# Performance work log

Hardware: AMD Instinct MI355X
Metric: run time of the kernel (lower is better)

## Reference

```python
import jax, jax.numpy as jnp
import numpy as np

BN_EPS = 1e-5


def _bn(x, g, b, m, v):
    # inference-mode BatchNorm1d over channel dim of [B, C, N]
    return g[:, None] * (x - m[:, None]) * jax.lax.rsqrt(v[:, None] + BN_EPS) + b[:, None]


def _conv1x1(w, x):
    # Conv1d kernel_size=1, no bias: [O, C] x [B, C, N] -> [B, O, N]
    return jnp.einsum('oc,bcn->bon', w, x)


def setup_inputs() -> dict:
    key = jax.random.key(0)
    ks = jax.random.split(key, 32)
    B, N = 8, 4096

    def w(k, sh):
        return jax.random.normal(k, sh, jnp.float32) * 0.05

    def bn_params(k, c):
        k0, k1, k2, k3 = jax.random.split(k, 4)
        g = 1.0 + 0.1 * jax.random.normal(k0, (c,), jnp.float32)
        b = 0.1 * jax.random.normal(k1, (c,), jnp.float32)
        m = 0.1 * jax.random.normal(k2, (c,), jnp.float32)
        v = jax.random.uniform(k3, (c,), jnp.float32, 0.5, 1.5)
        return g, b, m, v

    g1, b1, m1, v1 = bn_params(ks[2], 64)
    gq, bq, mq, vq = bn_params(ks[3], 16)
    gk, bk, mk, vk = bn_params(ks[4], 16)
    gv, bv, mv, vv = bn_params(ks[5], 3)

    return {
        'x': jax.random.normal(ks[0], (B, 3, N), jnp.float32),
        'w1': w(ks[6], (64, 3)),
        'g1': g1, 'b1': b1, 'm1': m1, 'v1': v1,
        'w2': w(ks[7], (128, 64)),
        'wq': w(ks[8], (16, 128)),
        'gq': gq, 'bq': bq, 'mq': mq, 'vq': vq,
        'wk': w(ks[9], (16, 128)),
        'gk': gk, 'bk': bk, 'mk': mk, 'vk': vk,
        'wv': w(ks[10], (3, 128)),
        'gv': gv, 'bv': bv, 'mv': mv, 'vv': vv,
        'alpha': 0.1 * jax.random.normal(ks[11], (1,), jnp.float32),
        'offset': 0.1 * jax.random.normal(ks[12], (1,), jnp.float32),
    }


def reference(x, w1, g1, b1, m1, v1, w2,
              wq, gq, bq, mq, vq,
              wk, gk, bk, mk, vk,
              wv, gv, bv, mv, vv,
              alpha, offset):
    # mlp: conv(3->64) -> BN -> ReLU -> conv(64->128)
    feat = _conv1x1(w2, jax.nn.relu(_bn(_conv1x1(w1, x + offset), g1, b1, m1, v1)))  # [B,128,N]
    q = jax.nn.relu(_bn(_conv1x1(wq, feat), gq, bq, mq, vq))  # [B,16,N]
    k = jax.nn.relu(_bn(_conv1x1(wk, feat), gk, bk, mk, vk))  # [B,16,N]
    energy = jnp.einsum('bcn,bcm->bnm', q, k)                 # [B,N,N] (Q^T K)
    sim = jax.nn.softmax(energy, axis=-1)
    # offset-attention: column-wise L1 renormalization
    sim = sim / (1e-9 + sim.sum(axis=1, keepdims=True))
    v_ = jax.nn.relu(_bn(_conv1x1(wv, feat), gv, bv, mv, vv))  # [B,3,N]
    out = jnp.einsum('bcn,bnm->bcm', v_, sim)                  # [B,3,N]
    return alpha * out + x
```

## Files before the change

### kernel.cpp

```cpp
#include <hip/hip_runtime.h>

#define NPTS 4096
#define NB   8
#define BN_EPS 1e-5f
#define LOG2E 1.4426950408889634f
#define RS_SLICES 8
#define CS_SLICES 4

typedef float f32x16 __attribute__((ext_vector_type(16)));
typedef short bf16x8 __attribute__((ext_vector_type(8)));
typedef unsigned short ushort_t;

#if __has_builtin(__builtin_amdgcn_exp2f)
#define EXP2(x) __builtin_amdgcn_exp2f(x)
#else
#define EXP2(x) exp2f(x)
#endif

__device__ __forceinline__ ushort_t f2bf(float f) {
    unsigned u = __builtin_bit_cast(unsigned, f);
    unsigned r = (u + 0x7FFFu + ((u >> 16) & 1u)) >> 16;
    return (ushort_t)r;
}

__global__ __launch_bounds__(256) void k0_prep(
    const float* __restrict__ w1, const float* __restrict__ g1, const float* __restrict__ b1,
    const float* __restrict__ m1, const float* __restrict__ v1,
    const float* __restrict__ w2,
    const float* __restrict__ wq, const float* __restrict__ gq, const float* __restrict__ bq,
    const float* __restrict__ mq, const float* __restrict__ vq,
    const float* __restrict__ wk, const float* __restrict__ gk, const float* __restrict__ bk,
    const float* __restrict__ mk, const float* __restrict__ vk,
    const float* __restrict__ wv, const float* __restrict__ gv, const float* __restrict__ bv,
    const float* __restrict__ mv, const float* __restrict__ vv,
    float* __restrict__ Wc, float* __restrict__ tb,
    float* __restrict__ w1s, float* __restrict__ t1)
{
    const int j = blockIdx.x;
    const int t = threadIdx.x;
    if (j == 35) {
        if (t < 64) {
            float s = g1[t] * rsqrtf(v1[t] + BN_EPS);
            w1s[t*3+0] = s * w1[t*3+0];
            w1s[t*3+1] = s * w1[t*3+1];
            w1s[t*3+2] = s * w1[t*3+2];
            t1[t] = b1[t] - s * m1[t];
        }
        return;
    }
    __shared__ float red[256];
    const int c = t & 63;
    const int chunk = t >> 6;
    const float* wrow;
    float g, bb, mm, vr, post = 1.f;
    if (j < 16)      { wrow = wq + j*128;      g = gq[j];    bb = bq[j];    mm = mq[j];    vr = vq[j];    post = LOG2E; }
    else if (j < 32) { int u = j-16; wrow = wk + u*128; g = gk[u]; bb = bk[u]; mm = mk[u]; vr = vk[u]; }
    else             { int u = j-32; wrow = wv + u*128; g = gv[u]; bb = bv[u]; mm = mv[u]; vr = vv[u]; }
    float acc = 0.f;
    for (int o = chunk*32; o < chunk*32 + 32; ++o) acc = fmaf(wrow[o], w2[o*64 + c], acc);
    red[t] = acc;
    __syncthreads();
    if (t < 64) {
        const float s4 = red[t] + red[64+t] + red[128+t] + red[192+t];
        const float sbn = g * rsqrtf(vr + BN_EPS);
        Wc[j*64 + t] = post * sbn * s4;
        if (t == 0) tb[j] = post * (bb - sbn * mm);
    }
}

__global__ __launch_bounds__(128) void k1_mlp(
    const float* __restrict__ x, const float* __restrict__ offset,
    const float* __restrict__ Wc, const float* __restrict__ tb,
    const float* __restrict__ w1s, const float* __restrict__ t1,
    ushort_t* __restrict__ qbuf, ushort_t* __restrict__ kbuf, float* __restrict__ aux)
{
    const int p = blockIdx.x*128 + threadIdx.x;
    const int b = p >> 12;
    const int n = p & 4095;
    const float off = offset[0];
    const float* xb = x + (size_t)b*3*NPTS + n;
    const float x0 = xb[0] + off, x1 = xb[NPTS] + off, x2 = xb[2*NPTS] + off;

    float acc[35];
#pragma unroll
    for (int j = 0; j < 35; ++j) acc[j] = tb[j];

    for (int c = 0; c < 64; ++c) {
        const float h = fmaxf(
            fmaf(w1s[c*3+0], x0, fmaf(w1s[c*3+1], x1, fmaf(w1s[c*3+2], x2, t1[c]))), 0.f);
        const float* wc = Wc + c;
#pragma unroll
        for (int j = 0; j < 35; ++j) acc[j] = fmaf(wc[j*64], h, acc[j]);
    }

    unsigned qw[8], kw[8];
#pragma unroll
    for (int i = 0; i < 8; ++i) {
        ushort_t qlo = f2bf(fmaxf(acc[2*i],    0.f));
        ushort_t qhi = f2bf(fmaxf(acc[2*i+1],  0.f));
        qw[i] = (unsigned)qlo | ((unsigned)qhi << 16);
        ushort_t klo = f2bf(fmaxf(acc[16+2*i],   0.f));
        ushort_t khi = f2bf(fmaxf(acc[16+2*i+1], 0.f));
        kw[i] = (unsigned)klo | ((unsigned)khi << 16);
    }
    uint4* qd = (uint4*)(qbuf + (size_t)p*16);
    qd[0] = make_uint4(qw[0], qw[1], qw[2], qw[3]);
    qd[1] = make_uint4(qw[4], qw[5], qw[6], qw[7]);
    uint4* kd = (uint4*)(kbuf + (size_t)p*16);
    kd[0] = make_uint4(kw[0], kw[1], kw[2], kw[3]);
    kd[1] = make_uint4(kw[4], kw[5], kw[6], kw[7]);
    float4* ar = (float4*)(aux + (size_t)p*4);
    *ar = make_float4(fmaxf(acc[32], 0.f), fmaxf(acc[33], 0.f), fmaxf(acc[34], 0.f), 0.f);
}

__global__ __launch_bounds__(256, 8) void k2_rowsum(
    const ushort_t* __restrict__ qbuf, const ushort_t* __restrict__ kbuf,
    float* __restrict__ psum)
{
    const int lane = threadIdx.x & 63;
    const int w = blockIdx.x*4 + (threadIdx.x >> 6);
    const int b = w >> 10;
    const int r = w & 1023;
    const int nblk = r >> 3;
    const int slice = r & 7;
    const int n0 = nblk * 32;
    const int m0 = slice * 512;

    const bf16x8 qfrag = *(const bf16x8*)(qbuf + ((size_t)b*NPTS + n0 + (lane & 31))*16 + (lane >> 5)*8);
    const ushort_t* kb = kbuf + ((size_t)b*NPTS + m0 + (lane & 31))*16 + (lane >> 5)*8;

    float rs0 = 0.f, rs1 = 0.f, rs2 = 0.f, rs3 = 0.f;
    bf16x8 kf0 = *(const bf16x8*)kb;
    bf16x8 kf1 = *(const bf16x8*)(kb + 512);
    for (int t = 0; t < 16; ++t) {
        const bf16x8 kcur = kf0;
        kf0 = kf1;
        const int tn = (t + 2 < 16) ? t + 2 : 15;
        kf1 = *(const bf16x8*)(kb + (size_t)tn*512);
        f32x16 acc;
#pragma unroll
        for (int i = 0; i < 16; ++i) acc[i] = 0.f;
        acc = __builtin_amdgcn_mfma_f32_32x32x16_bf16(kcur, qfrag, acc, 0, 0, 0);
#pragma unroll
        for (int i = 0; i < 16; i += 4) {
            rs0 += EXP2(acc[i+0]);
            rs1 += EXP2(acc[i+1]);
            rs2 += EXP2(acc[i+2]);
            rs3 += EXP2(acc[i+3]);
        }
    }
    float rsum = (rs0 + rs1) + (rs2 + rs3);
    rsum += __shfl_xor(rsum, 32);
    if (lane < 32) psum[((size_t)slice*NB + b)*NPTS + n0 + lane] = rsum;
}

__global__ __launch_bounds__(256) void k3_rowred(
    const float* __restrict__ psum, float* __restrict__ aux)
{
    const int p = blockIdx.x*256 + threadIdx.x;
    const int b = p >> 12;
    const int n = p & 4095;
    float s = 0.f;
#pragma unroll
    for (int sl = 0; sl < RS_SLICES; ++sl) s += psum[((size_t)sl*NB + b)*NPTS + n];
    const float inv = 1.0f / s;
    float4* ar = (float4*)(aux + (size_t)p*4);
    float4 v = *ar;
    *ar = make_float4(v.x*inv, v.y*inv, v.z*inv, inv);
}

__global__ __launch_bounds__(256, 4) void k4_colpass(
    const ushort_t* __restrict__ qbuf, const ushort_t* __restrict__ kbuf,
    const float* __restrict__ aux, float* __restrict__ pcol)
{
    const int lane = threadIdx.x & 63;
    const int w = blockIdx.x*4 + (threadIdx.x >> 6);
    const int b = w >> 9;
    const int r = w & 511;
    const int mtile = r >> 2;
    const int slice = r & 3;
    const int m0 = mtile * 32;
    const int n0 = slice * 1024;

    const bf16x8 afrag = *(const bf16x8*)(kbuf + ((size_t)b*NPTS + m0 + (lane & 31))*16 + (lane >> 5)*8);
    const ushort_t* qb = qbuf + ((size_t)b*NPTS + n0 + (lane & 31))*16 + (lane >> 5)*8;
    const float4* auxp = (const float4*)aux + (size_t)b*NPTS + n0 + (lane & 31);

    float S[16], A0[16], A1[16], A2[16];
#pragma unroll
    for (int i = 0; i < 16; ++i) { S[i] = 0.f; A0[i] = 0.f; A1[i] = 0.f; A2[i] = 0.f; }

    bf16x8 qf0 = *(const bf16x8*)qb;
    bf16x8 qf1 = *(const bf16x8*)(qb + 512);
    float4 ax0 = auxp[0];
    float4 ax1 = auxp[32];
    for (int t = 0; t < 32; ++t) {
        const bf16x8 qcur = qf0;
        const float4 axc = ax0;
        qf0 = qf1; ax0 = ax1;
        const int tn = (t + 2 < 32) ? t + 2 : 31;
        qf1 = *(const bf16x8*)(qb + (size_t)tn*512);
        ax1 = auxp[(size_t)tn*32];
        f32x16 acc;
#pragma unroll
        for (int i = 0; i < 16; ++i) acc[i] = 0.f;
        acc = __builtin_amdgcn_mfma_f32_32x32x16_bf16(afrag, qcur, acc, 0, 0, 0);
#pragma unroll
        for (int i = 0; i < 16; ++i) {
            const float e1 = EXP2(acc[i]);
            S[i]  = fmaf(axc.w, e1, S[i]);
            A0[i] = fmaf(axc.x, e1, A0[i]);
            A1[i] = fmaf(axc.y, e1, A1[i]);
            A2[i] = fmaf(axc.z, e1, A2[i]);
        }
    }

#pragma unroll
    for (int d = 1; d <= 16; d <<= 1) {
#pragma unroll
        for (int i = 0; i < 16; ++i) {
            S[i]  += __shfl_xor(S[i],  d);
            A0[i] += __shfl_xor(A0[i], d);
            A1[i] += __shfl_xor(A1[i], d);
            A2[i] += __shfl_xor(A2[i], d);
        }
    }

    if ((lane & 31) == 0) {
        const int hi = lane >> 5;
        float* base = pcol + (((size_t)b*CS_SLICES + slice)*4)*NPTS;
#pragma unroll
        for (int i = 0; i < 16; ++i) {
            const int m = m0 + (i & 3) + 8*(i >> 2) + 4*hi;
            base[0*NPTS + m] = S[i];
            base[1*NPTS + m] = A0[i];
            base[2*NPTS + m] = A1[i];
            base[3*NPTS + m] = A2[i];
        }
    }
}

__global__ __launch_bounds__(256) void k5_final(
    const float* __restrict__ pcol, const float* __restrict__ x,
    const float* __restrict__ alpha, float* __restrict__ out)
{
    const int p = blockIdx.x*256 + threadIdx.x;
    const int b = p >> 12;
    const int m = p & 4095;
    float s = 0.f, a0 = 0.f, a1 = 0.f, a2 = 0.f;
#pragma unroll
    for (int sl = 0; sl < CS_SLICES; ++sl) {
        const float* base = pcol + (((size_t)b*CS_SLICES + sl)*4)*NPTS;
        s  += base[0*NPTS + m];
        a0 += base[1*NPTS + m];
        a1 += base[2*NPTS + m];
        a2 += base[3*NPTS + m];
    }
    const float sc = alpha[0] / (1e-9f + s);
    const float* xb = x + (size_t)b*3*NPTS + m;
    float* ob = out + (size_t)b*3*NPTS + m;
    ob[0*NPTS] = fmaf(a0, sc, xb[0*NPTS]);
    ob[1*NPTS] = fmaf(a1, sc, xb[1*NPTS]);
    ob[2*NPTS] = fmaf(a2, sc, xb[2*NPTS]);
}

extern "C" void kernel_launch(void* const* d_in, const int* in_sizes, int n_in,
                              void* d_out, int out_size, void* d_ws, size_t ws_size,
                              hipStream_t stream) {
    const float* x      = (const float*)d_in[0];
    const float* w1     = (const float*)d_in[1];
    const float* g1     = (const float*)d_in[2];
    const float* b1     = (const float*)d_in[3];
    const float* m1     = (const float*)d_in[4];
    const float* v1     = (const float*)d_in[5];
    const float* w2     = (const float*)d_in[6];
    const float* wq     = (const float*)d_in[7];
    const float* gq     = (const float*)d_in[8];
    const float* bq     = (const float*)d_in[9];
    const float* mq     = (const float*)d_in[10];
    const float* vq     = (const float*)d_in[11];
    const float* wk     = (const float*)d_in[12];
    const float* gk     = (const float*)d_in[13];
    const float* bk     = (const float*)d_in[14];
    const float* mk     = (const float*)d_in[15];
    const float* vk     = (const float*)d_in[16];
    const float* wv     = (const float*)d_in[17];
    const float* gv     = (const float*)d_in[18];
    const float* bv     = (const float*)d_in[19];
    const float* mv     = (const float*)d_in[20];
    const float* vv     = (const float*)d_in[21];
    const float* alpha  = (const float*)d_in[22];
    const float* offset = (const float*)d_in[23];

    char* ws = (char*)d_ws;
    float*    Wc   = (float*)(ws + 0);
    float*    tb   = (float*)(ws + 16*1024);
    float*    w1s  = (float*)(ws + 32*1024);
    float*    t1   = (float*)(ws + 48*1024);
    ushort_t* qbuf = (ushort_t*)(ws + 64*1024);
    ushort_t* kbuf = (ushort_t*)(ws + 64*1024 + (size_t)1*1024*1024);
    float*    aux  = (float*)(ws + 64*1024 + (size_t)2*1024*1024);
    float*    psum = (float*)(ws + 64*1024 + (size_t)2*1024*1024 + 512*1024);
    float*    pcol = (float*)(ws + 64*1024 + (size_t)4*1024*1024);

    k0_prep<<<dim3(36), dim3(256), 0, stream>>>(
        w1, g1, b1, m1, v1, w2,
        wq, gq, bq, mq, vq,
        wk, gk, bk, mk, vk,
        wv, gv, bv, mv, vv,
        Wc, tb, w1s, t1);

    k1_mlp<<<dim3(256), dim3(128), 0, stream>>>(
        x, offset, Wc, tb, w1s, t1, qbuf, kbuf, aux);

    k2_rowsum<<<dim3(2048), dim3(256), 0, stream>>>(qbuf, kbuf, psum);
    k3_rowred<<<dim3(128), dim3(256), 0, stream>>>(psum, aux);
    k4_colpass<<<dim3(1024), dim3(256), 0, stream>>>(qbuf, kbuf, aux, pcol);
    k5_final<<<dim3(128), dim3(256), 0, stream>>>(pcol, x, alpha, (float*)d_out);
}
```

Baseline: 165.6 us.

## Split MLP channels across 4 lanes and fuse row-normalization into column pass

k1_mlp now assigns four threads per point, each handling 16 of the 64 hidden channels, and combines the partial sums with xor shuffles. This gives four times as many threads so the small, latency-bound kernel has more parallelism. k3_rowred is removed: each k4_colpass block reduces the row partial sums for its 1024-point n-slice, computes the reciprocal scale and stages the scaled aux values in LDS. The colpass then reads aux from LDS, saving a launch and a global round trip, but every m-group block of a slice recomputes the same row reductions.

```diff
diff --git a/kernel.cpp b/kernel.cpp
--- a/kernel.cpp
+++ b/kernel.cpp
@@ -68,13 +68,15 @@
     }
 }
 
-__global__ __launch_bounds__(128) void k1_mlp(
+__global__ __launch_bounds__(256) void k1_mlp(
     const float* __restrict__ x, const float* __restrict__ offset,
     const float* __restrict__ Wc, const float* __restrict__ tb,
     const float* __restrict__ w1s, const float* __restrict__ t1,
     ushort_t* __restrict__ qbuf, ushort_t* __restrict__ kbuf, float* __restrict__ aux)
 {
-    const int p = blockIdx.x*128 + threadIdx.x;
+    const int gt = blockIdx.x*256 + threadIdx.x;
+    const int p = gt >> 2;
+    const int sub = gt & 3;
     const int b = p >> 12;
     const int n = p & 4095;
     const float off = offset[0];
@@ -82,10 +84,18 @@
     const float x0 = xb[0] + off, x1 = xb[NPTS] + off, x2 = xb[2*NPTS] + off;
 
     float acc[35];
-#pragma unroll
-    for (int j = 0; j < 35; ++j) acc[j] = tb[j];
-
-    for (int c = 0; c < 64; ++c) {
+    if (sub == 0) {
+#pragma unroll
+        for (int j = 0; j < 35; ++j) acc[j] = tb[j];
+    } else {
+#pragma unroll
+        for (int j = 0; j < 35; ++j) acc[j] = 0.f;
+    }
+
+    const int c0 = sub * 16;
+#pragma unroll
+    for (int ci = 0; ci < 16; ++ci) {
+        const int c = c0 + ci;
         const float h = fmaxf(
             fmaf(w1s[c*3+0], x0, fmaf(w1s[c*3+1], x1, fmaf(w1s[c*3+2], x2, t1[c]))), 0.f);
         const float* wc = Wc + c;
@@ -93,24 +103,32 @@
         for (int j = 0; j < 35; ++j) acc[j] = fmaf(wc[j*64], h, acc[j]);
     }
 
-    unsigned qw[8], kw[8];
-#pragma unroll
-    for (int i = 0; i < 8; ++i) {
-        ushort_t qlo = f2bf(fmaxf(acc[2*i],    0.f));
-        ushort_t qhi = f2bf(fmaxf(acc[2*i+1],  0.f));
-        qw[i] = (unsigned)qlo | ((unsigned)qhi << 16);
-        ushort_t klo = f2bf(fmaxf(acc[16+2*i],   0.f));
-        ushort_t khi = f2bf(fmaxf(acc[16+2*i+1], 0.f));
-        kw[i] = (unsigned)klo | ((unsigned)khi << 16);
-    }
-    uint4* qd = (uint4*)(qbuf + (size_t)p*16);
-    qd[0] = make_uint4(qw[0], qw[1], qw[2], qw[3]);
-    qd[1] = make_uint4(qw[4], qw[5], qw[6], qw[7]);
-    uint4* kd = (uint4*)(kbuf + (size_t)p*16);
-    kd[0] = make_uint4(kw[0], kw[1], kw[2], kw[3]);
-    kd[1] = make_uint4(kw[4], kw[5], kw[6], kw[7]);
-    float4* ar = (float4*)(aux + (size_t)p*4);
-    *ar = make_float4(fmaxf(acc[32], 0.f), fmaxf(acc[33], 0.f), fmaxf(acc[34], 0.f), 0.f);
+#pragma unroll
+    for (int j = 0; j < 35; ++j) {
+        acc[j] += __shfl_xor(acc[j], 1);
+        acc[j] += __shfl_xor(acc[j], 2);
+    }
+
+    if (sub == 0) {
+        unsigned qw[8], kw[8];
+#pragma unroll
+        for (int i = 0; i < 8; ++i) {
+            ushort_t qlo = f2bf(fmaxf(acc[2*i],    0.f));
+            ushort_t qhi = f2bf(fmaxf(acc[2*i+1],  0.f));
+            qw[i] = (unsigned)qlo | ((unsigned)qhi << 16);
+            ushort_t klo = f2bf(fmaxf(acc[16+2*i],   0.f));
+            ushort_t khi = f2bf(fmaxf(acc[16+2*i+1], 0.f));
+            kw[i] = (unsigned)klo | ((unsigned)khi << 16);
+        }
+        uint4* qd = (uint4*)(qbuf + (size_t)p*16);
+        qd[0] = make_uint4(qw[0], qw[1], qw[2], qw[3]);
+        qd[1] = make_uint4(qw[4], qw[5], qw[6], qw[7]);
+        uint4* kd = (uint4*)(kbuf + (size_t)p*16);
+        kd[0] = make_uint4(kw[0], kw[1], kw[2], kw[3]);
+        kd[1] = make_uint4(kw[4], kw[5], kw[6], kw[7]);
+        float4* ar = (float4*)(aux + (size_t)p*4);
+        *ar = make_float4(fmaxf(acc[32], 0.f), fmaxf(acc[33], 0.f), fmaxf(acc[34], 0.f), 0.f);
+    }
 }
 
 __global__ __launch_bounds__(256, 8) void k2_rowsum(
@@ -154,37 +172,40 @@
     if (lane < 32) psum[((size_t)slice*NB + b)*NPTS + n0 + lane] = rsum;
 }
 
-__global__ __launch_bounds__(256) void k3_rowred(
-    const float* __restrict__ psum, float* __restrict__ aux)
-{
-    const int p = blockIdx.x*256 + threadIdx.x;
-    const int b = p >> 12;
-    const int n = p & 4095;
-    float s = 0.f;
-#pragma unroll
-    for (int sl = 0; sl < RS_SLICES; ++sl) s += psum[((size_t)sl*NB + b)*NPTS + n];
-    const float inv = 1.0f / s;
-    float4* ar = (float4*)(aux + (size_t)p*4);
-    float4 v = *ar;
-    *ar = make_float4(v.x*inv, v.y*inv, v.z*inv, inv);
-}
-
 __global__ __launch_bounds__(256, 4) void k4_colpass(
     const ushort_t* __restrict__ qbuf, const ushort_t* __restrict__ kbuf,
-    const float* __restrict__ aux, float* __restrict__ pcol)
-{
-    const int lane = threadIdx.x & 63;
-    const int w = blockIdx.x*4 + (threadIdx.x >> 6);
-    const int b = w >> 9;
-    const int r = w & 511;
-    const int mtile = r >> 2;
-    const int slice = r & 3;
+    const float* __restrict__ aux, const float* __restrict__ psum,
+    float* __restrict__ pcol)
+{
+    __shared__ float4 s_ax[1024];
+
+    const int tid  = threadIdx.x;
+    const int lane = tid & 63;
+    const int widx = tid >> 6;
+    const int blk  = blockIdx.x;
+    const int b      = blk >> 7;
+    const int slice  = (blk >> 5) & 3;
+    const int mgroup = blk & 31;
+    const int mtile  = mgroup*4 + widx;
     const int m0 = mtile * 32;
     const int n0 = slice * 1024;
 
+#pragma unroll
+    for (int i = 0; i < 4; ++i) {
+        const int nl = tid + i*256;
+        const int gn = n0 + nl;
+        float s = 0.f;
+#pragma unroll
+        for (int sl = 0; sl < RS_SLICES; ++sl)
+            s += psum[((size_t)sl*NB + b)*NPTS + gn];
+        const float inv = 1.0f / s;
+        const float4 v = *((const float4*)aux + (size_t)b*NPTS + gn);
+        s_ax[nl] = make_float4(v.x*inv, v.y*inv, v.z*inv, inv);
+    }
+    __syncthreads();
+
     const bf16x8 afrag = *(const bf16x8*)(kbuf + ((size_t)b*NPTS + m0 + (lane & 31))*16 + (lane >> 5)*8);
     const ushort_t* qb = qbuf + ((size_t)b*NPTS + n0 + (lane & 31))*16 + (lane >> 5)*8;
-    const float4* auxp = (const float4*)aux + (size_t)b*NPTS + n0 + (lane & 31);
 
     float S[16], A0[16], A1[16], A2[16];
 #pragma unroll
@@ -192,15 +213,12 @@
 
     bf16x8 qf0 = *(const bf16x8*)qb;
     bf16x8 qf1 = *(const bf16x8*)(qb + 512);
-    float4 ax0 = auxp[0];
-    float4 ax1 = auxp[32];
     for (int t = 0; t < 32; ++t) {
         const bf16x8 qcur = qf0;
-        const float4 axc = ax0;
-        qf0 = qf1; ax0 = ax1;
+        qf0 = qf1;
         const int tn = (t + 2 < 32) ? t + 2 : 31;
         qf1 = *(const bf16x8*)(qb + (size_t)tn*512);
-        ax1 = auxp[(size_t)tn*32];
+        const float4 axc = s_ax[(lane & 31) + t*32];
         f32x16 acc;
 #pragma unroll
         for (int i = 0; i < 16; ++i) acc[i] = 0.f;
@@ -310,11 +328,10 @@
         wv, gv, bv, mv, vv,
         Wc, tb, w1s, t1);
 
-    k1_mlp<<<dim3(256), dim3(128), 0, stream>>>(
+    k1_mlp<<<dim3(512), dim3(256), 0, stream>>>(
         x, offset, Wc, tb, w1s, t1, qbuf, kbuf, aux);
 
     k2_rowsum<<<dim3(2048), dim3(256), 0, stream>>>(qbuf, kbuf, psum);
-    k3_rowred<<<dim3(128), dim3(256), 0, stream>>>(psum, aux);
-    k4_colpass<<<dim3(1024), dim3(256), 0, stream>>>(qbuf, kbuf, aux, pcol);
+    k4_colpass<<<dim3(1024), dim3(256), 0, stream>>>(qbuf, kbuf, aux, psum, pcol);
     k5_final<<<dim3(128), dim3(256), 0, stream>>>(pcol, x, alpha, (float*)d_out);
 }
```

Result: slower. 174.2 us (+5.2%).
